# Optimization experiments

Measured on AMD Instinct MI355X. Metric: run time of the kernel, lower is better.

## Reference

```python
import jax, jax.numpy as jnp
import numpy as np

L = 524288      # input_length (~33 s @ 16 kHz)
C = 129         # cochlear channels
DS = 80         # downsample rate = sr / (1000 / frame_length)


def setup_inputs() -> dict:
    key = jax.random.key(0)
    k0, k1, k2 = jax.random.split(key, 3)
    x = jax.random.normal(k0, (L,), dtype=jnp.float32)
    # Filterbank transfer functions (stand-in for cochlear_filter_params.npz)
    Hs_real = 0.1 * jax.random.normal(k1, (C, L), dtype=jnp.float32)
    Hs_imag = 0.1 * jax.random.normal(k2, (C, L), dtype=jnp.float32)
    alpha_comp = jnp.full((C,), 0.9, dtype=jnp.float32)
    alpha_leak = jnp.array(0.9922179, dtype=jnp.float32)
    li_kernel = jnp.array([1.0, -1.0], dtype=jnp.float32)  # first-difference conv kernel
    return {"x": x, "Hs_real": Hs_real, "Hs_imag": Hs_imag,
            "alpha_comp": alpha_comp, "alpha_leak": alpha_leak,
            "li_kernel": li_kernel}


def reference(x, Hs_real, Hs_imag, alpha_comp, alpha_leak, li_kernel):
    # 1. Cochlear filterbank: FFT -> per-channel complex multiply -> IFFT
    X = jnp.fft.fft(x)                                   # [L] complex
    Hs = Hs_real + 1j * Hs_imag                          # [C, L]
    coch = jnp.fft.ifft(Hs * X[None, :], axis=-1).real   # [C, L]

    # 2. Power-law compression per channel: |x|^a * sign(x)
    comp = jnp.abs(coch) ** alpha_comp[:, None] * jnp.sign(coch)

    # 3-4. LIN: first difference along channel axis (SAME pad -> zero row at end), then ReLU
    shifted = jnp.concatenate([comp[1:], jnp.zeros_like(comp[:1])], axis=0)
    lin = jax.nn.relu(comp * li_kernel[0] + shifted * li_kernel[1])

    # 5. Leaky integration via FFT-domain filtering, then downsample
    freqs = jnp.fft.fftfreq(L).astype(jnp.float32) * (2.0 * jnp.pi)
    Hleak = 1.0 / (1.0 - alpha_leak * (jnp.cos(freqs) - 1j * jnp.sin(freqs)))  # [L]
    out = jnp.fft.ifft(Hleak[None, :] * jnp.fft.fft(lin, axis=-1), axis=-1).real
    return out[:, DS - 1::DS]                            # [C, L // DS]
```

## Files before the change

### kernel.cpp

```cpp
#include <hip/hip_runtime.h>
#include <math.h>

#define LN    524288
#define N1    512
#define N2    1024
#define NCH   129
#define DSR   80
#define NOUT  6553
#define OB2   64
#define NBLK  103
#define SPB   (OB2*DSR)
#define TPW   20
#define NPAIR 65
#define KTAIL 48
#define SB    1024
#define LMAP(i) ((i) + ((i) >> 3))
#define SWZ(p)  ((p) ^ ((((p) >> 5) & 1) * 31))

__device__ __forceinline__ float2 cmulf(float2 a, float2 b) {
    return make_float2(a.x*b.x - a.y*b.y, a.x*b.y + a.y*b.x);
}

__device__ __forceinline__ float powsign(float x, float a) {
    float m = __builtin_amdgcn_exp2f(a * __builtin_amdgcn_logf(fabsf(x)));
    return copysignf(m, x);
}

__global__ void pack_x(const float* __restrict__ x, float2* __restrict__ dst) {
    int i = blockIdx.x * 256 + threadIdx.x;
    dst[i] = make_float2(x[i], 0.f);
}

__global__ void transpose_c(const float2* __restrict__ src, float2* __restrict__ dst,
                            int R, int Cc) {
    __shared__ float2 tile[32][33];
    size_t boff = (size_t)blockIdx.z * LN;
    src += boff; dst += boff;
    int x  = blockIdx.x * 32 + threadIdx.x;
    int y0 = blockIdx.y * 32 + threadIdx.y;
#pragma unroll
    for (int i = 0; i < 32; i += 8)
        tile[threadIdx.y + i][threadIdx.x] = src[(size_t)(y0 + i) * Cc + x];
    __syncthreads();
    int xo  = blockIdx.y * 32 + threadIdx.x;
    int yo0 = blockIdx.x * 32 + threadIdx.y;
#pragma unroll
    for (int i = 0; i < 32; i += 8)
        dst[(size_t)(yo0 + i) * R + xo] = tile[threadIdx.x][threadIdx.y + i];
}

template<int M, int SIGN, int TW>
__global__ __launch_bounds__(256) void fft_rows(const float2* __restrict__ src,
                                                float2* __restrict__ dst,
                                                int rows_per_batch) {
    __shared__ __align__(16) float2 ping[M];
    __shared__ __align__(16) float2 pong[M];
    __shared__ float2 twid[M];
    size_t rowg = blockIdx.x;
    const float2* srow = src + rowg * M;
    float2* drow = dst + rowg * M;
    int row = (int)(rowg % (size_t)rows_per_batch);
    int t = threadIdx.x;
    const float4* s4 = (const float4*)srow;
    for (int ii = t; ii < M/2; ii += 256)
        *(float4*)&ping[2*ii] = s4[ii];
    for (int i = t; i < M; i += 256) {
        if (i >= 1) {
            int h = 1 << (31 - __clz((unsigned)i));
            float ang = (float)SIGN * 3.14159265358979323846f * (float)(i - h) / (float)h;
            float s, c; __sincosf(ang, &s, &c);
            twid[i] = make_float2(c, s);
        }
    }
    __syncthreads();
    float2* a = ping;
    float2* b = pong;
    for (int Ns = 1; Ns < M; Ns <<= 1) {
        for (int j = t; j < M/2; j += 256) {
            int jm = j & (Ns - 1);
            float2 v0 = a[j];
            float2 v1 = a[j + M/2];
            float2 tw = twid[Ns + jm];
            float2 w = make_float2(v1.x*tw.x - v1.y*tw.y, v1.x*tw.y + v1.y*tw.x);
            int d0 = ((j & ~(Ns - 1)) << 1) | jm;
            b[d0]      = make_float2(v0.x + w.x, v0.y + w.y);
            b[d0 + Ns] = make_float2(v0.x - w.x, v0.y - w.y);
        }
        __syncthreads();
        float2* tmp = a; a = b; b = tmp;
    }
    if (TW) {
        const float c2pi = 6.28318530717958647692f / (float)LN;
        for (int i = t; i < M; i += 256) {
            float2 v = a[i];
            unsigned prod = ((unsigned)row * (unsigned)i) & (unsigned)(LN - 1);
            float ang = (float)SIGN * c2pi * (float)prod;
            float s, c;
            __sincosf(ang, &s, &c);
            drow[i] = make_float2(v.x*c - v.y*s, v.x*s + v.y*c);
        }
    } else {
        float4* d4 = (float4*)drow;
        for (int ii = t; ii < M/2; ii += 256)
            d4[ii] = *(const float4*)&a[2*ii];
    }
}

__device__ __forceinline__ void herm2(float2 X1,
                                      float har,  float hai,  float hbr,  float hbi,
                                      float har2, float hai2, float hbr2, float hbi2,
                                      bool hasB, float2& Wk, float2& WkL) {
    float2 a1 = make_float2(har*X1.x - hai*X1.y, har*X1.y + hai*X1.x);
    float2 a2 = make_float2(har2*X1.x + hai2*X1.y, hai2*X1.x - har2*X1.y);
    float yar = 0.5f*(a1.x + a2.x), yai = 0.5f*(a1.y - a2.y);
    float ybr = 0.f, ybi = 0.f;
    if (hasB) {
        float2 b1 = make_float2(hbr*X1.x - hbi*X1.y, hbr*X1.y + hbi*X1.x);
        float2 b2 = make_float2(hbr2*X1.x + hbi2*X1.y, hbi2*X1.x - hbr2*X1.y);
        ybr = 0.5f*(b1.x + b2.x); ybi = 0.5f*(b1.y - b2.y);
    }
    Wk  = make_float2(yar - ybi, yai + ybr);
    WkL = make_float2(yar + ybi, ybr - yai);
}

__global__ __launch_bounds__(256) void build_w6(const float* __restrict__ Hr,
                                                const float* __restrict__ Hi,
                                                const float2* __restrict__ X,
                                                float2* __restrict__ W, int pair0) {
    __shared__ float mirS[4][1160];
    int s0 = blockIdx.x * SB;
    int pl = blockIdx.y;
    int p  = pair0 + pl;
    int ca = 2*p, cb = 2*p + 1;
    bool hasB = (cb < NCH);
    const float* Hs0 = Hr + (size_t)ca * LN;
    const float* Hs1 = Hi + (size_t)ca * LN;
    const float* Hs2 = hasB ? (Hr + (size_t)cb * LN) : Hs0;
    const float* Hs3 = hasB ? (Hi + (size_t)cb * LN) : Hs1;
    const float* Hs[4] = {Hs0, Hs1, Hs2, Hs3};
    float2* Wp = W + (size_t)pl * LN;
    int t = threadIdx.x;
    int j4 = 4 * t;
    int mbase = LN - s0 - SB;

    float4 lowv[4];
#pragma unroll
    for (int a = 0; a < 4; a++) {
        lowv[a] = *(const float4*)&Hs[a][s0 + j4];
        float4 mv = *(const float4*)&Hs[a][mbase + j4];
        int lm = LMAP(j4);
        mirS[a][lm+0] = mv.x; mirS[a][lm+1] = mv.y; mirS[a][lm+2] = mv.z; mirS[a][lm+3] = mv.w;
    }
    if (t == 1 && s0 > 0) {
#pragma unroll
        for (int a = 0; a < 4; a++) mirS[a][LMAP(SB)] = Hs[a][LN - s0];
    }
    float nxt[4];
#pragma unroll
    for (int a = 0; a < 4; a++) nxt[a] = __shfl_down(lowv[a].x, 1);
    if ((t & 63) == 63) {
#pragma unroll
        for (int a = 0; a < 4; a++) nxt[a] = Hs[a][s0 + j4 + 4];
    }
    __syncthreads();

    float4 xa = *(const float4*)&X[s0 + j4];
    float4 xb = *(const float4*)&X[s0 + j4 + 2];
    float2 wlo[4];
#pragma unroll
    for (int d = 0; d < 4; d++) {
        int k = s0 + j4 + d;
        float2 Xk = (d == 0) ? make_float2(xa.x, xa.y) :
                    (d == 1) ? make_float2(xa.z, xa.w) :
                    (d == 2) ? make_float2(xb.x, xb.y) : make_float2(xb.z, xb.w);
        float hl[4] = { (d==0)?lowv[0].x:(d==1)?lowv[0].y:(d==2)?lowv[0].z:lowv[0].w,
                        (d==0)?lowv[1].x:(d==1)?lowv[1].y:(d==2)?lowv[1].z:lowv[1].w,
                        (d==0)?lowv[2].x:(d==1)?lowv[2].y:(d==2)?lowv[2].z:lowv[2].w,
                        (d==0)?lowv[3].x:(d==1)?lowv[3].y:(d==2)?lowv[3].z:lowv[3].w };
        if (k == 0) {
            float2 Ya = cmulf(make_float2(hl[0], hl[1]), Xk);
            float br = 0.f;
            if (hasB) { float2 Yb = cmulf(make_float2(hl[2], hl[3]), Xk); br = Yb.x; }
            wlo[d] = make_float2(Ya.x, br);
        } else {
            int jm = LMAP(SB - j4 - d);
            float2 Wk, WkL;
            herm2(Xk, hl[0], hl[1], hl[2], hl[3],
                      mirS[0][jm], mirS[1][jm], mirS[2][jm], mirS[3][jm], hasB, Wk, WkL);
            wlo[d] = Wk;
        }
    }
    *(float4*)&Wp[s0 + j4]     = make_float4(wlo[0].x, wlo[0].y, wlo[1].x, wlo[1].y);
    *(float4*)&Wp[s0 + j4 + 2] = make_float4(wlo[2].x, wlo[2].y, wlo[3].x, wlo[3].y);

    int e0 = SB - 4 - j4;
    float2 wmi[4];
#pragma unroll
    for (int d = 0; d < 4; d++) {
        int ee = e0 + d;
        int m  = mbase + ee;
        int jm = LMAP(ee);
        if (m == LN/2) {
            float2 Xv = X[LN/2];
            float2 Ya = cmulf(make_float2(mirS[0][jm], mirS[1][jm]), Xv);
            float br = 0.f;
            if (hasB) { float2 Yb = cmulf(make_float2(mirS[2][jm], mirS[3][jm]), Xv); br = Yb.x; }
            wmi[d] = make_float2(Ya.x, br);
        } else {
            int kp = LN - m;
            float hl[4];
#pragma unroll
            for (int a = 0; a < 4; a++)
                hl[a] = (d==0) ? nxt[a] : (d==1) ? lowv[a].w : (d==2) ? lowv[a].z : lowv[a].y;
            float2 Xk = X[kp];
            float2 Wk, WkL;
            herm2(Xk, hl[0], hl[1], hl[2], hl[3],
                      mirS[0][jm], mirS[1][jm], mirS[2][jm], mirS[3][jm], hasB, Wk, WkL);
            wmi[d] = WkL;
        }
    }
    *(float4*)&Wp[mbase + e0]     = make_float4(wmi[0].x, wmi[0].y, wmi[1].x, wmi[1].y);
    *(float4*)&Wp[mbase + e0 + 2] = make_float4(wmi[2].x, wmi[2].y, wmi[3].x, wmi[3].y);
}

#define R4_BFLY(SRE, SIM, P, H, Q, TWID)                                        \
    {                                                                            \
        float2 W1 = TWID[2*(H) + (Q)];                                           \
        float2 W2 = TWID[(H) + (Q)];                                             \
        float2 W3 = cmulf(W1, W2);                                               \
        int p0 = SWZ(P), p1 = SWZ((P) + (H)), p2 = SWZ((P) + 2*(H)), p3 = SWZ((P) + 3*(H)); \
        float x0r = SRE[p0], x0i = SIM[p0];                                      \
        float x1r = SRE[p1], x1i = SIM[p1];                                      \
        float x2r = SRE[p2], x2i = SIM[p2];                                      \
        float x3r = SRE[p3], x3i = SIM[p3];                                      \
        float s02r = x0r + x2r, s02i = x0i + x2i;                                \
        float d02r = x0r - x2r, d02i = x0i - x2i;                                \
        float s13r = x1r + x3r, s13i = x1i + x3i;                                \
        float d13r = x1r - x3r, d13i = x1i - x3i;                                \
        SRE[p0] = s02r + s13r;  SIM[p0] = s02i + s13i;                           \
        float ar = s02r - s13r, ai = s02i - s13i;                                \
        SRE[p1] = ar*W2.x - ai*W2.y;  SIM[p1] = ar*W2.y + ai*W2.x;               \
        float br = d02r - d13i, bi = d02i + d13r;                                \
        SRE[p2] = br*W1.x - bi*W1.y;  SIM[p2] = br*W1.y + bi*W1.x;               \
        float cr = d02r + d13i, ci = d02i - d13r;                                \
        SRE[p3] = cr*W3.x - ci*W3.y;  SIM[p3] = cr*W3.y + ci*W3.x;               \
    }

__global__ __launch_bounds__(1024) void kB(float2* __restrict__ D1) {
    __shared__ float sRe[16][545];
    __shared__ float sIm[16][545];
    __shared__ float2 twid[512];
    int cg = blockIdx.x;
    int pl = blockIdx.y;
    float2* Dp = D1 + (size_t)pl * LN;
    unsigned c_base = 16u * cg;
    int t = threadIdx.x;

    if (t >= 1 && t < 512) {
        int h = 1 << (31 - __clz((unsigned)t));
        float ang = 3.14159265358979323846f * (float)(t - h) / (float)h;
        float s, c; __sincosf(ang, &s, &c);
        twid[t] = make_float2(c, s);
    }

    int cc = t & 15;
    int g  = (t >> 4) & 3;
    int w  = t >> 6;

#pragma unroll
    for (int i = 0; i < 8; i++) {
        int r = w + (g << 4) + (i << 6);
        float2 v = Dp[(size_t)r * N2 + c_base + cc];
        int sp = SWZ(r);
        sRe[cc][sp] = v.x;
        sIm[cc][sp] = v.y;
    }
    __syncthreads();

    int cc2 = t >> 6;
    int l   = t & 63;
    float* re = sRe[cc2];
    float* im = sIm[cc2];
    for (int H = 128; H >= 2; H >>= 2) {
#pragma unroll
        for (int i = 0; i < 2; i++) {
            int u = l + (i << 6);
            int q = u & (H - 1);
            int p = ((u & ~(H - 1)) << 2) | q;
            R4_BFLY(re, im, p, H, q, twid);
        }
        __syncthreads();
    }
#pragma unroll
    for (int i = 0; i < 4; i++) {
        int j = l + (i << 6);
        int p0 = SWZ(2*j), p1 = SWZ(2*j + 1);
        float ar = re[p0], ai = im[p0];
        float br = re[p1], bi = im[p1];
        re[p0] = ar + br;  im[p0] = ai + bi;
        re[p1] = ar - br;  im[p1] = ai - bi;
    }
    __syncthreads();

    const float c2pi = 6.28318530717958647692f / (float)LN;
    unsigned truec = c_base + (unsigned)cc;
#pragma unroll
    for (int i = 0; i < 8; i++) {
        int pos = w + (g << 4) + (i << 6);
        unsigned jj = __brev((unsigned)pos) >> 23;
        int sp = SWZ(pos);
        float rr = sRe[cc][sp], ii = sIm[cc][sp];
        unsigned prod = (jj * truec) & (unsigned)(LN - 1);
        float ang = c2pi * (float)prod;
        float s, c;
        __sincosf(ang, &s, &c);
        Dp[(size_t)jj * N2 + truec] = make_float2(rr*c - ii*s, rr*s + ii*c);
    }
}

__global__ __launch_bounds__(512) void kC(const float2* __restrict__ D1,
                                          float* __restrict__ comp,
                                          const float* __restrict__ alpha_comp,
                                          int pair0) {
    __shared__ float sRe[8][1057];
    __shared__ float sIm[8][1057];
    __shared__ float2 twid[1024];
    int rg = blockIdx.x;
    int pl = blockIdx.y;
    int p  = pair0 + pl;
    int ca = 2*p, cb = 2*p + 1;
    const float2* Dp = D1 + (size_t)pl * LN;
    int jj0 = rg * 8;
    int t = threadIdx.x;
    for (int i = t; i < 1024; i += 512) {
        if (i >= 1) {
            int h = 1 << (31 - __clz((unsigned)i));
            float ang = 3.14159265358979323846f * (float)(i - h) / (float)h;
            float s, c; __sincosf(ang, &s, &c);
            twid[i] = make_float2(c, s);
        }
    }
    int w = t >> 6, l = t & 63;

    const float4* rowp = (const float4*)(Dp + (size_t)(jj0 + w) * N2);
#pragma unroll
    for (int i = 0; i < 8; i++) {
        int q4 = l + (i << 6);
        float4 v = rowp[q4];
        int a0 = SWZ(2*q4), a1 = SWZ(2*q4 + 1);
        sRe[w][a0] = v.x; sIm[w][a0] = v.y;
        sRe[w][a1] = v.z; sIm[w][a1] = v.w;
    }
    __syncthreads();

    float* re = sRe[w];
    float* im = sIm[w];
    for (int H = 256; H >= 1; H >>= 2) {
#pragma unroll
        for (int i = 0; i < 4; i++) {
            int u = l + (i << 6);
            int q = u & (H - 1);
            int p4 = ((u & ~(H - 1)) << 2) | q;
            R4_BFLY(re, im, p4, H, q, twid);
        }
        __syncthreads();
    }

    float aa = alpha_comp[ca];
    float ab = (cb < NCH) ? alpha_comp[cb] : 1.f;
    const float invL = 1.f / (float)LN;
    int r  = t & 7;
    int dm = (t >> 3) & 7;
#pragma unroll
    for (int i = 0; i < 16; i++) {
        int m = (w << 7) + (i << 3) + dm;
        unsigned pp = __brev((unsigned)m) >> 22;
        int sp = SWZ((int)pp);
        float rr = sRe[r][sp] * invL;
        float ii = sIm[r][sp] * invL;
        size_t n = (size_t)m * N1 + jj0 + r;
        comp[(size_t)ca * LN + n] = powsign(rr, aa);
        if (cb < NCH)
            comp[(size_t)cb * LN + n] = powsign(ii, ab);
    }
}

__global__ __launch_bounds__(256) void iir_part1(
    const float* __restrict__ comp, const float* __restrict__ alpha_leak,
    const float* __restrict__ li_kernel, float* __restrict__ out,
    float* __restrict__ carryOut) {
    __shared__ float win[SPB + SPB/TPW];
    __shared__ float wv[4], wg[4];
    int blk = blockIdx.x;
    int c = blockIdx.y;
    int t = threadIdx.x;
    float alpha = alpha_leak[0];
    float k0 = li_kernel[0], k1 = li_kernel[1];
    int base = blk * SPB;
    const int cap = NOUT * DSR;
    const float* c0 = comp + (size_t)c * LN;
    const float* c1 = (c + 1 < NCH) ? comp + (size_t)(c + 1) * LN : nullptr;
    const float4 z4 = make_float4(0.f, 0.f, 0.f, 0.f);
    for (int i4 = 4*t; i4 < SPB; i4 += 1024) {
        int g = base + i4;
        float4 u0 = *(const float4*)&c0[g];
        float4 u1 = c1 ? *(const float4*)&c1[g] : z4;
        float vv[4] = {k0*u0.x + k1*u1.x, k0*u0.y + k1*u1.y,
                       k0*u0.z + k1*u1.z, k0*u0.w + k1*u1.w};
#pragma unroll
        for (int d = 0; d < 4; d++) {
            float v = fmaxf(vv[d], 0.f);
            if (g + d >= cap) v = 0.f;
            int i = i4 + d;
            win[i + i / TPW] = v;
        }
    }
    __syncthreads();
    float v = 0.f;
    int lbase = 21 * t;
#pragma unroll
    for (int i = 0; i < TPW; i++)
        v = fmaf(alpha, v, win[lbase + i]);
    float g = powf(alpha, (float)TPW);
    int lid = t & 63, wid = t >> 6;
#pragma unroll
    for (int d = 1; d < 64; d <<= 1) {
        float pv = __shfl_up(v, d);
        float pg = __shfl_up(g, d);
        if (lid >= d) { v = fmaf(g, pv, v); g = g * pg; }
    }
    if (lid == 63) { wv[wid] = v; wg[wid] = g; }
    __syncthreads();
    float cv = 0.f;
#pragma unroll
    for (int w = 0; w < 3; w++)
        if (w < wid) cv = wv[w] + wg[w] * cv;
    float vf = fmaf(g, cv, v);
    int nact = NOUT - blk * OB2; if (nact > OB2) nact = OB2;
    if ((t & 3) == 3) {
        int o = t >> 2;
        if (o < nact)
            out[(size_t)c * NOUT + blk * OB2 + o] = vf;
    }
    if (t == 4 * nact - 1)
        carryOut[c * NBLK + blk] = vf;
}

__global__ void iir_part2(const float* __restrict__ comp, const float* __restrict__ alpha_leak,
                          const float* __restrict__ li_kernel,
                          const float* __restrict__ carryOut, float* __restrict__ D) {
    int c = threadIdx.x;
    if (c >= NCH) return;
    float alpha = alpha_leak[0];
    float k0 = li_kernel[0], k1 = li_kernel[1];
    const float* c0 = comp + (size_t)c * LN;
    const float* c1 = (c + 1 < NCH) ? comp + (size_t)(c + 1) * LN : nullptr;
    float tail = 0.f, ap = 1.f;
    for (int j = 0; j < KTAIL; j++) {
        int g = LN - 1 - j;
        float u0 = c0[g];
        float u1 = c1 ? c1[g] : 0.f;
        float v = k0 * u0 + k1 * u1; v = v > 0.f ? v : 0.f;
        tail += ap * v;
        ap *= alpha;
    }
    float D0 = tail + ap * carryOut[c * NBLK + (NBLK - 1)]
             + powf(alpha, (float)(KTAIL + 2000)) * carryOut[c * NBLK + (NBLK - 2)];
    D[c * NBLK + 0] = D0;
    for (int b = 1; b < NBLK; b++)
        D[c * NBLK + b] = carryOut[c * NBLK + b - 1];
}

__global__ void iir_part3(const float* __restrict__ D, const float* __restrict__ alpha_leak,
                          float* __restrict__ out) {
    int idx = blockIdx.x * 256 + threadIdx.x;
    if (idx >= NCH * NOUT) return;
    int c = idx / NOUT, m = idx - c * NOUT;
    int b = m / OB2, o = m - b * OB2;
    float alpha = alpha_leak[0];
    float beta = powf(alpha, (float)DSR);
    float dec = powf(beta, (float)(o + 1));
    out[idx] += dec * D[c * NBLK + b];
}

extern "C" void kernel_launch(void* const* d_in, const int* in_sizes, int n_in,
                              void* d_out, int out_size, void* d_ws, size_t ws_size,
                              hipStream_t stream) {
    const float* x  = (const float*)d_in[0];
    const float* Hr = (const float*)d_in[1];
    const float* Hi = (const float*)d_in[2];
    const float* ac = (const float*)d_in[3];
    const float* al = (const float*)d_in[4];
    const float* li = (const float*)d_in[5];
    float* out = (float*)d_out;

    char* ws = (char*)d_ws;
    size_t off = 0;
    auto alloc = [&](size_t bytes) -> void* {
        void* p = ws + off;
        off += (bytes + 255) & ~(size_t)255;
        return p;
    };
    float2* Xf     = (float2*)alloc((size_t)LN * sizeof(float2));
    float*  comp   = (float*) alloc((size_t)NCH * LN * sizeof(float));
    float*  cOut   = (float*) alloc((size_t)NCH * NBLK * sizeof(float));
    float*  Dbuf   = (float*) alloc((size_t)NCH * NBLK * sizeof(float));
    size_t remain = (ws_size > off) ? (ws_size - off) : 0;
    int chunk = (int)(remain / ((size_t)LN * sizeof(float2)));
    if (chunk > NPAIR) chunk = NPAIR;
    if (chunk < 2)     chunk = 2;
    float2* bufA = (float2*)alloc((size_t)chunk * LN * sizeof(float2));

    dim3 tb(32, 8, 1);

    float2* fA = bufA;
    float2* fB = bufA + LN;
    pack_x<<<LN / 256, 256, 0, stream>>>(x, fA);
    transpose_c<<<dim3(N2/32, N1/32, 1), tb, 0, stream>>>(fA, fB, N1, N2);
    fft_rows<N1, -1, 1><<<N2, 256, 0, stream>>>(fB, fB, N2);
    transpose_c<<<dim3(N1/32, N2/32, 1), tb, 0, stream>>>(fB, fA, N2, N1);
    fft_rows<N2, -1, 0><<<N1, 256, 0, stream>>>(fA, fA, N1);
    transpose_c<<<dim3(N2/32, N1/32, 1), tb, 0, stream>>>(fA, Xf, N1, N2);

    for (int ci = 0; ci < NPAIR; ci += chunk) {
        int np = NPAIR - ci; if (np > chunk) np = chunk;
        build_w6<<<dim3(LN/2/SB, np), 256, 0, stream>>>(Hr, Hi, Xf, bufA, ci);
        kB<<<dim3(64, np), 1024, 0, stream>>>(bufA);
        kC<<<dim3(64, np), 512, 0, stream>>>(bufA, comp, ac, ci);
    }

    iir_part1<<<dim3(NBLK, NCH, 1), 256, 0, stream>>>(comp, al, li, out, cOut);
    iir_part2<<<1, 256, 0, stream>>>(comp, al, li, cOut, Dbuf);
    iir_part3<<<(NCH * NOUT + 255) / 256, 256, 0, stream>>>(Dbuf, al, out);
}
```

Measured before the change: 635.6 us.

## Compute kC row FFT in registers with wavefront shuffles instead of LDS radix-4

Replaces the shared-memory radix-4 1024-point FFT in kC with a register-resident decimation-in-frequency FFT. Each lane holds 16 points; the first four stages run within registers and the last six use cross-lane shuffles. Results are written to LDS only once, before the bit-reversed output read. This removes repeated LDS traffic and block-wide barriers between stages, at the cost of more registers and many shuffle instructions.

```diff
diff --git a/kernel.cpp b/kernel.cpp
--- a/kernel.cpp
+++ b/kernel.cpp
@@ -318,6 +318,23 @@
     }
 }
 
+#define REG_STAGE(HR, H)                                                        \
+    {                                                                            \
+        _Pragma("unroll")                                                        \
+        for (int u = 0; u < 8; u++) {                                            \
+            int qr = u & ((HR) - 1);                                             \
+            int b0 = ((u & ~((HR) - 1)) << 1) | qr;                              \
+            int b1 = b0 + (HR);                                                  \
+            float2 tw = twid[(H) + (qr << 6) + l];                               \
+            float ar = vRe[b0], ai = vIm[b0];                                    \
+            float br = vRe[b1], bi = vIm[b1];                                    \
+            vRe[b0] = ar + br;  vIm[b0] = ai + bi;                               \
+            float dr = ar - br, di = ai - bi;                                    \
+            vRe[b1] = dr*tw.x - di*tw.y;                                         \
+            vIm[b1] = dr*tw.y + di*tw.x;                                         \
+        }                                                                        \
+    }
+
 __global__ __launch_bounds__(512) void kC(const float2* __restrict__ D1,
                                           float* __restrict__ comp,
                                           const float* __restrict__ alpha_comp,
@@ -342,29 +359,45 @@
     }
     int w = t >> 6, l = t & 63;
 
-    const float4* rowp = (const float4*)(Dp + (size_t)(jj0 + w) * N2);
-#pragma unroll
-    for (int i = 0; i < 8; i++) {
-        int q4 = l + (i << 6);
-        float4 v = rowp[q4];
-        int a0 = SWZ(2*q4), a1 = SWZ(2*q4 + 1);
-        sRe[w][a0] = v.x; sIm[w][a0] = v.y;
-        sRe[w][a1] = v.z; sIm[w][a1] = v.w;
-    }
-    __syncthreads();
-
-    float* re = sRe[w];
-    float* im = sIm[w];
-    for (int H = 256; H >= 1; H >>= 2) {
-#pragma unroll
-        for (int i = 0; i < 4; i++) {
-            int u = l + (i << 6);
-            int q = u & (H - 1);
-            int p4 = ((u & ~(H - 1)) << 2) | q;
-            R4_BFLY(re, im, p4, H, q, twid);
-        }
-        __syncthreads();
-    }
+    float vRe[16], vIm[16];
+    const float2* row2 = Dp + (size_t)(jj0 + w) * N2;
+#pragma unroll
+    for (int r = 0; r < 16; r++) {
+        float2 v = row2[(r << 6) + l];
+        vRe[r] = v.x; vIm[r] = v.y;
+    }
+    __syncthreads();
+
+    REG_STAGE(8, 512)
+    REG_STAGE(4, 256)
+    REG_STAGE(2, 128)
+    REG_STAGE(1, 64)
+
+#pragma unroll
+    for (int h = 32; h >= 1; h >>= 1) {
+        float2 tw = twid[h + (l & (h - 1))];
+        bool up = (l & h) == 0;
+#pragma unroll
+        for (int r = 0; r < 16; r++) {
+            float oR = __shfl_xor(vRe[r], h);
+            float oI = __shfl_xor(vIm[r], h);
+            float sR = vRe[r] + oR;
+            float sI = vIm[r] + oI;
+            float dr = oR - vRe[r], di = oI - vIm[r];
+            float dR = dr*tw.x - di*tw.y;
+            float dI = dr*tw.y + di*tw.x;
+            vRe[r] = up ? sR : dR;
+            vIm[r] = up ? sI : dI;
+        }
+    }
+
+#pragma unroll
+    for (int r = 0; r < 16; r++) {
+        int sp = SWZ((r << 6) + l);
+        sRe[w][sp] = vRe[r];
+        sIm[w][sp] = vIm[r];
+    }
+    __syncthreads();
 
     float aa = alpha_comp[ca];
     float ab = (cb < NCH) ? alpha_comp[cb] : 1.f;
```

Result: no change. 638.6 us (+0.5%).
